# Kernel tuning notes

Hardware: AMD Instinct MI355X
Metric: run time of the kernel (lower is better)

## Reference

```python
import jax, jax.numpy as jnp
import numpy as np

KS, PH, PW, SH, SW = 3, 1, 1, 1, 1


def setup_inputs() -> dict:
    key = jax.random.key(0)
    k1, k2, k3 = jax.random.split(key, 3)
    bs, p_in, H, W = 8, 64, 64, 64
    p_out = 64
    vs = KS * KS + 1
    x = jax.random.normal(k1, (bs, p_in, H, W), dtype=jnp.float32)
    # kaiming-uniform-like init scale for filters (fan_in = p_in*vs*vs)
    fan_in = p_in * vs * vs
    bound = float(np.sqrt(6.0 / fan_in))
    filters = jax.random.uniform(k2, (p_out, p_in, vs, vs), dtype=jnp.float32,
                                 minval=-bound, maxval=bound)
    biases = jax.random.uniform(k3, (p_out,), dtype=jnp.float32, minval=-1.0, maxval=1.0)
    return {"x": x, "filters": filters, "biases": biases}


def reference(x, filters, biases):
    # x: (bs, p_in, H, W); filters: (p_out, p_in, vs, vs); biases: (p_out,)
    bs, p_in = x.shape[0], x.shape[1]
    p_out = filters.shape[0]
    vs = KS * KS + 1
    # Extract ks x ks patches -> (bs, p_in*ks*ks, Ho, Wo), feature dim ordered (C, kh, kw)
    patches = jax.lax.conv_general_dilated_patches(
        x, filter_shape=(KS, KS), window_strides=(SH, SW),
        padding=[(PH, PH), (PW, PW)])
    Ho, Wo = patches.shape[-2], patches.shape[-1]
    P = patches.reshape(bs, p_in, KS * KS, Ho, Wo)
    # Prepend constant 1 -> augmented patch vector s of length vs (matches torch cat(ones, spot))
    ones = jnp.ones((bs, p_in, 1, Ho, Wo), dtype=x.dtype)
    S = jnp.concatenate([ones, P], axis=2)            # (bs, p_in, vs, Ho, Wo)
    # Move pixels to a single leading dim: (M, p_in, vs) with M = bs*Ho*Wo
    S = S.transpose(0, 3, 4, 1, 2).reshape(bs * Ho * Wo, p_in, vs)
    # Per-pixel, per-channel outer product s s^T: (M, p_in, vs, vs)
    Q = S[:, :, :, None] * S[:, :, None, :]
    # Quadratic form contraction with filters as one GEMM:
    # out[m, o] = sum_{c,i,j} Q[m,c,i,j] * filters[o,c,i,j]
    out = Q.reshape(bs * Ho * Wo, p_in * vs * vs) @ filters.reshape(p_out, -1).T
    out = out + biases[None, :]
    return out.reshape(bs, Ho, Wo, p_out).transpose(0, 3, 1, 2)
```

## Files before the change

### kernel.cpp

```cpp
#include <hip/hip_runtime.h>
#include <stdint.h>

#define HH 64
#define WW 64
#define PIN 64
#define POUT 64
#define NFEAT 54

typedef _Float16 half8 __attribute__((ext_vector_type(8)));
typedef _Float16 half4 __attribute__((ext_vector_type(4)));
typedef float f32x4 __attribute__((ext_vector_type(4)));
typedef float f32x16 __attribute__((ext_vector_type(16)));

__constant__ const int KT[54] = {0,0,0,0,0,0,0,0,0, 1,1,1,1,1,1,1,1,1, 2,2,2,2,2,2,2,2,
                                 3,3,3,3,3,3,3, 4,4,4,4,4,4, 5,5,5,5,5, 6,6,6,6, 7,7,7, 8,8, 9};
__constant__ const int LT[54] = {1,2,3,4,5,6,7,8,9, 1,2,3,4,5,6,7,8,9, 2,3,4,5,6,7,8,9,
                                 3,4,5,6,7,8,9, 4,5,6,7,8,9, 5,6,7,8,9, 6,7,8,9, 7,8,9, 8,9, 9};

__global__ void prep_filters(const float* __restrict__ f, const float* __restrict__ bias,
                             _Float16* __restrict__ fprep, float* __restrict__ fconst) {
    if (blockIdx.x == 108) {
        int o = threadIdx.x;
        if (o < POUT) {
            float s = bias[o];
            for (int c = 0; c < PIN; ++c) s += f[(size_t)(o * PIN + c) * 100];
            fconst[o] = s;
        }
        return;
    }
    int tid = blockIdx.x * 256 + threadIdx.x;
    int feat = tid >> 9;
    int rem = tid & 511;
    int o = rem >> 3;
    int cg = rem & 7;
    int k = KT[feat], l = LT[feat];

    half8 chunk;
    #pragma unroll
    for (int jj = 0; jj < 8; ++jj) {
        int c = cg * 8 + jj;
        const float* fc = f + (size_t)(o * PIN + c) * 100;
        float v;
        if (k == 0)      v = fc[l] + fc[l * 10];
        else if (k == l) v = fc[k * 10 + k];
        else             v = fc[k * 10 + l] + fc[l * 10 + k];
        chunk[jj] = (_Float16)v;
    }
    int lane = (o & 31) + 32 * (cg & 1);
    size_t byte = (size_t)feat * 8192 + (cg >> 1) * 2048 + (o >> 5) * 1024 + lane * 16;
    *(half8*)((char*)fprep + byte) = chunk;
}

__global__ __launch_bounds__(512, 4) void poly2d_mfma(
    const float* __restrict__ x, const _Float16* __restrict__ fprep,
    const float* __restrict__ fconst, float* __restrict__ out)
{
    __shared__ __align__(16) char smx[25344];

    const int t = threadIdx.x;
    const int lane = t & 63;
    const int wid = t >> 6;
    const int bid = (blockIdx.x & 7) * 64 + (blockIdx.x >> 3);
    const int b = bid >> 6;
    const int hrow = bid & 63;

    {
        const int w = t & 63;
        const int wl = w + 1;
        #pragma unroll
        for (int h = 0; h < 3; ++h) {
            int h_in = hrow - 1 + h;
            bool hok = ((unsigned)h_in < HH);
            #pragma unroll
            for (int cc = 0; cc < 2; ++cc) {
                int c = wid * 8 + cc * 4;
                float v0 = 0.f, v1 = 0.f, v2 = 0.f, v3 = 0.f;
                if (hok) {
                    const float* gx = x + (((size_t)b * PIN + c) * HH + h_in) * WW + w;
                    v0 = gx[0]; v1 = gx[4096]; v2 = gx[8192]; v3 = gx[12288];
                }
                half4 pk = {(_Float16)v0, (_Float16)v1, (_Float16)v2, (_Float16)v3};
                int byte = ((h * 66 + wl) * 8 + ((c >> 3) ^ (wl & 7))) * 16 + (c & 7) * 2;
                *(half4*)(smx + byte) = pk;
            }
        }
        if (t < 48) {
            int h = t >> 4, side = (t >> 3) & 1, cg = t & 7;
            int wl2 = side ? 65 : 0;
            int byte = ((h * 66 + wl2) * 8 + (cg ^ (wl2 & 7))) * 16;
            f32x4 z = {0.f, 0.f, 0.f, 0.f};
            *(f32x4*)(smx + byte) = z;
        }
    }
    __syncthreads();

    const int kc = wid >> 1;
    const int mwid = wid & 1;
    const int wbase = mwid * 32;
    const int l31 = lane & 31;
    const int lhi = lane >> 5;

    half8 xp[9];
    #pragma unroll
    for (int p = 1; p <= 9; ++p) {
        const int dh = (p - 1) / 3 - 1, dw = (p - 1) % 3 - 1;
        int wl = wbase + l31 + dw + 1;
        int hidx = dh + 1;
        int cgl = kc * 2 + lhi;
        int byte = ((hidx * 66 + wl) * 8 + (cgl ^ (wl & 7))) * 16;
        xp[p - 1] = *(const half8*)(smx + byte);
    }
    __syncthreads();

    const char* fbase = (const char*)fprep + (kc << 11) + (lane << 4);

    half8 Bb[4][2];
    #pragma unroll
    for (int s = 0; s < 3; ++s) {
        Bb[s][0] = *(const half8*)(fbase + (size_t)s * 8192);
        Bb[s][1] = *(const half8*)(fbase + (size_t)s * 8192 + 1024);
    }

    f32x16 acc0 = {}, acc1 = {};

    #pragma unroll
    for (int f = 0; f < NFEAT; ++f) {
        if (f + 3 < NFEAT) {
            Bb[(f + 3) & 3][0] = *(const half8*)(fbase + (size_t)(f + 3) * 8192);
            Bb[(f + 3) & 3][1] = *(const half8*)(fbase + (size_t)(f + 3) * 8192 + 1024);
        }
        const int k = KT[f], l = LT[f];
        half8 a = (k == 0) ? xp[l - 1] : xp[k - 1] * xp[l - 1];
        acc0 = __builtin_amdgcn_mfma_f32_32x32x16_f16(a, Bb[f & 3][0], acc0, 0, 0, 0);
        acc1 = __builtin_amdgcn_mfma_f32_32x32x16_f16(a, Bb[f & 3][1], acc1, 0, 0, 0);
    }

    __syncthreads();
    float* os = (float*)smx;

    #pragma unroll
    for (int pass = 0; pass < 4; ++pass) {
        if (kc == pass) {
            #pragma unroll
            for (int nb = 0; nb < 2; ++nb) {
                #pragma unroll
                for (int r = 0; r < 16; ++r) {
                    int row = (r & 3) + 8 * (r >> 2) + 4 * lhi;
                    int m = mwid * 32 + row;
                    int col = l31 + nb * 32;
                    float v = nb ? acc1[r] : acc0[r];
                    if (pass == 0) os[m * 65 + col] = v;
                    else           os[m * 65 + col] += v;
                }
            }
        }
        __syncthreads();
    }

    {
        const int w = t & 63;
        #pragma unroll
        for (int oo = 0; oo < 8; ++oo) {
            int o = wid * 8 + oo;
            float val = os[w * 65 + o] + fconst[o];
            out[(((size_t)b * POUT + o) * HH + hrow) * WW + w] = val;
        }
    }
}

__global__ __launch_bounds__(256) void poly2d_fp32(
    const float* __restrict__ x, const float* __restrict__ f,
    const float* __restrict__ bias, float* __restrict__ out)
{
    const int t = threadIdx.x;
    const int wo = t & 63;
    const int ho = (blockIdx.x & 15) * 4 + (t >> 6);
    const int o = (blockIdx.x >> 4) & 63;
    const int b = blockIdx.x >> 10;

    float acc = bias[o];
    const float* xb = x + (size_t)b * PIN * HH * WW;
    const float* fo = f + (size_t)o * PIN * 100;
    for (int c = 0; c < PIN; ++c) {
        const float* xc = xb + (size_t)c * HH * WW;
        float s[10];
        s[0] = 1.0f;
        #pragma unroll
        for (int kh = 0; kh < 3; ++kh) {
            int h = ho - 1 + kh;
            bool hok = ((unsigned)h < HH);
            #pragma unroll
            for (int kw = 0; kw < 3; ++kw) {
                int w = wo - 1 + kw;
                s[1 + kh * 3 + kw] = (hok && (unsigned)w < WW) ? xc[h * WW + w] : 0.0f;
            }
        }
        const float* fc = fo + c * 100;
        #pragma unroll
        for (int i = 0; i < 10; ++i) {
            float wsum = 0.0f;
            #pragma unroll
            for (int j = 0; j < 10; ++j) wsum = fmaf(fc[i * 10 + j], s[j], wsum);
            acc = fmaf(wsum, s[i], acc);
        }
    }
    out[(((size_t)b * POUT + o) * HH + ho) * WW + wo] = acc;
}

extern "C" void kernel_launch(void* const* d_in, const int* in_sizes, int n_in,
                              void* d_out, int out_size, void* d_ws, size_t ws_size,
                              hipStream_t stream) {
    const float* x    = (const float*)d_in[0];
    const float* filt = (const float*)d_in[1];
    const float* bias = (const float*)d_in[2];
    float* out = (float*)d_out;

    const size_t FPREP_BYTES = (size_t)NFEAT * POUT * PIN * 2;
    if (ws_size < FPREP_BYTES + 256) {
        poly2d_fp32<<<dim3(8 * 64 * 16), dim3(256), 0, stream>>>(x, filt, bias, out);
        return;
    }
    _Float16* fprep = (_Float16*)d_ws;
    float* fconst = (float*)((char*)d_ws + FPREP_BYTES);

    prep_filters<<<dim3(109), dim3(256), 0, stream>>>(filt, bias, fprep, fconst);
    poly2d_mfma<<<dim3(512), dim3(512), 0, stream>>>(x, fprep, fconst, out);
}
```

Measured before the change: 29.69 us.

## Process two output rows per block to reuse filter fragments across rows

Each block now computes two output rows instead of one, loading four input rows into shared memory and running four MFMA accumulators per wave so each loaded filter fragment feeds two row tiles. This halves the per-block filter global loads relative to output and shares the halo row, at the cost of higher register pressure (launch bounds lowered to 2 blocks), more LDS, and only 256 blocks on a 256-CU device, leaving one block per CU and less latency hiding.

```diff
diff --git a/kernel.cpp b/kernel.cpp
--- a/kernel.cpp
+++ b/kernel.cpp
@@ -51,25 +51,25 @@
     *(half8*)((char*)fprep + byte) = chunk;
 }
 
-__global__ __launch_bounds__(512, 4) void poly2d_mfma(
+__global__ __launch_bounds__(512, 2) void poly2d_mfma(
     const float* __restrict__ x, const _Float16* __restrict__ fprep,
     const float* __restrict__ fconst, float* __restrict__ out)
 {
-    __shared__ __align__(16) char smx[25344];
+    __shared__ __align__(16) char smx[33792];
 
     const int t = threadIdx.x;
     const int lane = t & 63;
     const int wid = t >> 6;
-    const int bid = (blockIdx.x & 7) * 64 + (blockIdx.x >> 3);
-    const int b = bid >> 6;
-    const int hrow = bid & 63;
+    const int bid = (blockIdx.x & 7) * 32 + (blockIdx.x >> 3);
+    const int b = bid >> 5;
+    const int rp = bid & 31;
 
     {
         const int w = t & 63;
         const int wl = w + 1;
         #pragma unroll
-        for (int h = 0; h < 3; ++h) {
-            int h_in = hrow - 1 + h;
+        for (int h = 0; h < 4; ++h) {
+            int h_in = rp * 2 - 1 + h;
             bool hok = ((unsigned)h_in < HH);
             #pragma unroll
             for (int cc = 0; cc < 2; ++cc) {
@@ -84,8 +84,8 @@
                 *(half4*)(smx + byte) = pk;
             }
         }
-        if (t < 48) {
-            int h = t >> 4, side = (t >> 3) & 1, cg = t & 7;
+        if (t < 64) {
+            int h = t & 3, side = (t >> 2) & 1, cg = t >> 3;
             int wl2 = side ? 65 : 0;
             int byte = ((h * 66 + wl2) * 8 + (cg ^ (wl2 & 7))) * 16;
             f32x4 z = {0.f, 0.f, 0.f, 0.f};
@@ -95,20 +95,22 @@
     __syncthreads();
 
     const int kc = wid >> 1;
-    const int mwid = wid & 1;
-    const int wbase = mwid * 32;
+    const int ms = wid & 1;
     const int l31 = lane & 31;
     const int lhi = lane >> 5;
 
-    half8 xp[9];
+    half8 xp[9][2];
     #pragma unroll
     for (int p = 1; p <= 9; ++p) {
         const int dh = (p - 1) / 3 - 1, dw = (p - 1) % 3 - 1;
-        int wl = wbase + l31 + dw + 1;
-        int hidx = dh + 1;
-        int cgl = kc * 2 + lhi;
-        int byte = ((hidx * 66 + wl) * 8 + (cgl ^ (wl & 7))) * 16;
-        xp[p - 1] = *(const half8*)(smx + byte);
+        #pragma unroll
+        for (int j = 0; j < 2; ++j) {
+            int wl = ms * 32 + l31 + dw + 1;
+            int hidx = j + dh + 1;
+            int cgl = kc * 2 + lhi;
+            int byte = ((hidx * 66 + wl) * 8 + (cgl ^ (wl & 7))) * 16;
+            xp[p - 1][j] = *(const half8*)(smx + byte);
+        }
     }
     __syncthreads();
 
@@ -121,7 +123,7 @@
         Bb[s][1] = *(const half8*)(fbase + (size_t)s * 8192 + 1024);
     }
 
-    f32x16 acc0 = {}, acc1 = {};
+    f32x16 acc00 = {}, acc01 = {}, acc10 = {}, acc11 = {};
 
     #pragma unroll
     for (int f = 0; f < NFEAT; ++f) {
@@ -130,9 +132,12 @@
             Bb[(f + 3) & 3][1] = *(const half8*)(fbase + (size_t)(f + 3) * 8192 + 1024);
         }
         const int k = KT[f], l = LT[f];
-        half8 a = (k == 0) ? xp[l - 1] : xp[k - 1] * xp[l - 1];
-        acc0 = __builtin_amdgcn_mfma_f32_32x32x16_f16(a, Bb[f & 3][0], acc0, 0, 0, 0);
-        acc1 = __builtin_amdgcn_mfma_f32_32x32x16_f16(a, Bb[f & 3][1], acc1, 0, 0, 0);
+        half8 a0 = (k == 0) ? xp[l - 1][0] : xp[k - 1][0] * xp[l - 1][0];
+        half8 a1 = (k == 0) ? xp[l - 1][1] : xp[k - 1][1] * xp[l - 1][1];
+        acc00 = __builtin_amdgcn_mfma_f32_32x32x16_f16(a0, Bb[f & 3][0], acc00, 0, 0, 0);
+        acc01 = __builtin_amdgcn_mfma_f32_32x32x16_f16(a0, Bb[f & 3][1], acc01, 0, 0, 0);
+        acc10 = __builtin_amdgcn_mfma_f32_32x32x16_f16(a1, Bb[f & 3][0], acc10, 0, 0, 0);
+        acc11 = __builtin_amdgcn_mfma_f32_32x32x16_f16(a1, Bb[f & 3][1], acc11, 0, 0, 0);
     }
 
     __syncthreads();
@@ -142,15 +147,19 @@
     for (int pass = 0; pass < 4; ++pass) {
         if (kc == pass) {
             #pragma unroll
-            for (int nb = 0; nb < 2; ++nb) {
+            for (int j = 0; j < 2; ++j) {
                 #pragma unroll
-                for (int r = 0; r < 16; ++r) {
-                    int row = (r & 3) + 8 * (r >> 2) + 4 * lhi;
-                    int m = mwid * 32 + row;
-                    int col = l31 + nb * 32;
-                    float v = nb ? acc1[r] : acc0[r];
-                    if (pass == 0) os[m * 65 + col] = v;
-                    else           os[m * 65 + col] += v;
+                for (int nb = 0; nb < 2; ++nb) {
+                    #pragma unroll
+                    for (int r = 0; r < 16; ++r) {
+                        int midx = (r & 3) + 8 * (r >> 2) + 4 * lhi;
+                        int px = j * 64 + ms * 32 + midx;
+                        int col = l31 + nb * 32;
+                        float v = (j == 0) ? (nb ? acc01[r] : acc00[r])
+                                           : (nb ? acc11[r] : acc10[r]);
+                        if (pass == 0) os[px * 65 + col] = v;
+                        else           os[px * 65 + col] += v;
+                    }
                 }
             }
         }
@@ -160,10 +169,13 @@
     {
         const int w = t & 63;
         #pragma unroll
-        for (int oo = 0; oo < 8; ++oo) {
-            int o = wid * 8 + oo;
-            float val = os[w * 65 + o] + fconst[o];
-            out[(((size_t)b * POUT + o) * HH + hrow) * WW + w] = val;
+        for (int h2 = 0; h2 < 2; ++h2) {
+            #pragma unroll
+            for (int oo = 0; oo < 8; ++oo) {
+                int o = wid * 8 + oo;
+                float val = os[(h2 * 64 + w) * 65 + o] + fconst[o];
+                out[(((size_t)b * POUT + o) * HH + (rp * 2 + h2)) * WW + w] = val;
+            }
         }
     }
 }
@@ -224,5 +236,5 @@
     float* fconst = (float*)((char*)d_ws + FPREP_BYTES);
 
     prep_filters<<<dim3(109), dim3(256), 0, stream>>>(filt, bias, fprep, fconst);
-    poly2d_mfma<<<dim3(512), dim3(512), 0, stream>>>(x, fprep, fconst, out);
-}
+    poly2d_mfma<<<dim3(256), dim3(512), 0, stream>>>(x, fprep, fconst, out);
+}
```

New measurement: 32.09 us. 1.08x slower.
